# Performance work log

Hardware: AMD Instinct MI355X
Metric: run time of the kernel (lower is better)

## Reference

```python
import jax, jax.numpy as jnp
import numpy as np


def setup_inputs() -> dict:
    key = jax.random.key(0)
    k1, k2 = jax.random.split(key)
    B, H, W, D = 2, 160, 192, 160
    X = jax.random.normal(k1, (B, H, W, D, 2), dtype=jnp.float32)
    deformation = jax.random.normal(k2, (B, H, W, D, 3), dtype=jnp.float32)
    return {"X": X, "deformation": deformation}


def reference(X, deformation):
    # X: (B,H,W,D,2); warp the first channel by the dense deformation field.
    B, H, W, D, _ = X.shape
    Y = X[..., 0:1]                     # (B,H,W,D,1) volume to warp
    N = H * W * D

    # Identity grid, matching tf.meshgrid(x,y,z) 'xy' semantics: shape (H,W,D),
    # x varies along axis1 (width), y along axis0 (height), z along axis2 (depth).
    ys, xs, zs = jnp.meshgrid(
        jnp.arange(H, dtype=jnp.float32),
        jnp.arange(W, dtype=jnp.float32),
        jnp.arange(D, dtype=jnp.float32),
        indexing='ij')

    d = deformation.reshape(B, N, 3)
    x = xs.reshape(-1)[None, :] + d[..., 0]   # (B,N)
    y = ys.reshape(-1)[None, :] + d[..., 1]
    z = zs.reshape(-1)[None, :] + d[..., 2]

    x0 = jnp.floor(x).astype(jnp.int32); x1 = x0 + 1
    y0 = jnp.floor(y).astype(jnp.int32); y1 = y0 + 1
    z0 = jnp.floor(z).astype(jnp.int32); z1 = z0 + 1

    x0 = jnp.clip(x0, 0, W - 1); x1 = jnp.clip(x1, 0, W - 1)
    y0 = jnp.clip(y0, 0, H - 1); y1 = jnp.clip(y1, 0, H - 1)
    z0 = jnp.clip(z0, 0, D - 1); z1 = jnp.clip(z1, 0, D - 1)

    flat = Y.reshape(B, N, 1)           # (B, H*W*D, C=1)

    def gather(yy, xx, zz):
        idx = (yy * (W * D) + xx * D + zz)[..., None]   # (B,N,1)
        return jnp.take_along_axis(flat, idx, axis=1)

    p000 = gather(y0, x0, z0); p001 = gather(y0, x0, z1)
    p010 = gather(y0, x1, z0); p011 = gather(y0, x1, z1)
    p100 = gather(y1, x0, z0); p101 = gather(y1, x0, z1)
    p110 = gather(y1, x1, z0); p111 = gather(y1, x1, z1)

    # Weights use the CLIPPED corner coordinates (faithful to the original).
    x0f = x0.astype(jnp.float32); x1f = x1.astype(jnp.float32)
    y0f = y0.astype(jnp.float32); y1f = y1.astype(jnp.float32)
    z0f = z0.astype(jnp.float32); z1f = z1.astype(jnp.float32)

    w000 = ((y1f - y) * (x1f - x) * (z1f - z))[..., None]
    w001 = ((y1f - y) * (x1f - x) * (z - z0f))[..., None]
    w010 = ((y1f - y) * (x - x0f) * (z1f - z))[..., None]
    w011 = ((y1f - y) * (x - x0f) * (z - z0f))[..., None]
    w100 = ((y - y0f) * (x1f - x) * (z1f - z))[..., None]
    w101 = ((y - y0f) * (x1f - x) * (z - z0f))[..., None]
    w110 = ((y - y0f) * (x - x0f) * (z1f - z))[..., None]
    w111 = ((y - y0f) * (x - x0f) * (z - z0f))[..., None]

    out = (w000 * p000 + w001 * p001 + w010 * p010 + w011 * p011 +
           w100 * p100 + w101 * p101 + w110 * p110 + w111 * p111)
    return out.reshape(B, H, W, D, 1)
```

## Files before the change

### kernel.cpp

```cpp
#include <hip/hip_runtime.h>

#define BB 2
#define HH 160
#define WW 192
#define DD 160
#define NN (HH * WW * DD)
#define TOTAL (BB * NN)

__device__ inline unsigned short f2bf(float f) {
    unsigned u = __builtin_bit_cast(unsigned, f);
    u += 0x7FFFu + ((u >> 16) & 1u);
    return (unsigned short)(u >> 16);
}
__device__ inline float bf2f_lo(unsigned v) {
    return __builtin_bit_cast(float, v << 16);
}
__device__ inline float bf2f_hi(unsigned v) {
    return __builtin_bit_cast(float, v & 0xFFFF0000u);
}

struct __attribute__((packed, aligned(8))) f6u { float a, b, c, d, e, f; };

__global__ __launch_bounds__(256)
void compact_ch0_bf16_kernel(const float4* __restrict__ X4,
                             ushort4* __restrict__ C4) {
    const int i = blockIdx.x * 256 + threadIdx.x;
    const float4 a = X4[4 * i];
    const float4 b = X4[4 * i + 1];
    const float4 c = X4[4 * i + 2];
    const float4 d = X4[4 * i + 3];
    ushort4 lo, hi;
    lo.x = f2bf(a.x); lo.y = f2bf(a.z); lo.z = f2bf(b.x); lo.w = f2bf(b.z);
    hi.x = f2bf(c.x); hi.y = f2bf(c.z); hi.z = f2bf(d.x); hi.w = f2bf(d.z);
    C4[2 * i]     = lo;
    C4[2 * i + 1] = hi;
}

__global__ __launch_bounds__(256, 6)
void SpatialDeformer3D_kernel(const unsigned short* __restrict__ C,
                              const float* __restrict__ def,
                              float* __restrict__ out) {
    const int t  = blockIdx.x * 256 + threadIdx.x;
    const int n0 = t * 2;

    const int b    = (n0 >= NN) ? 1 : 0;
    const int rem  = n0 - b * NN;
    const int h    = rem / (WW * DD);
    const int rem2 = rem - h * (WW * DD);
    const int w    = rem2 / DD;
    const int d0   = rem2 - w * DD;

    const f6u dv = *(const f6u*)(def + (size_t)n0 * 3);
    const float dxs[2] = {dv.a, dv.d};
    const float dys[2] = {dv.b, dv.e};
    const float dzs[2] = {dv.c, dv.f};

    const unsigned bbase = (unsigned)b * (unsigned)NN * 2u;

    float xs[2], ys[2], zs[2];
    int aix0[2], aix1[2], aiy0[2], aiy1[2], alo[2], ahi[2], azb[2];
    unsigned o0, o1, o2, o3, o4, o5, o6, o7;
#pragma unroll
    for (int k = 0; k < 2; ++k) {
        const float x = (float)w + dxs[k];
        const float y = (float)h + dys[k];
        const float z = (float)(d0 + k) + dzs[k];
        xs[k] = x; ys[k] = y; zs[k] = z;

        const int fx0 = (int)floorf(x);
        const int fy0 = (int)floorf(y);
        const int fz0 = (int)floorf(z);

        const int ix0 = min(max(fx0, 0), WW - 1), ix1 = min(max(fx0 + 1, 0), WW - 1);
        const int iy0 = min(max(fy0, 0), HH - 1), iy1 = min(max(fy0 + 1, 0), HH - 1);
        const int czlo = min(max(fz0, 0), DD - 1);
        const int czhi = min(max(fz0 + 1, 0), DD - 1);
        const int zb   = min(max(fz0, 0), DD - 2);

        aix0[k] = ix0; aix1[k] = ix1; aiy0[k] = iy0; aiy1[k] = iy1;
        alo[k] = czlo; ahi[k] = czhi; azb[k] = zb;

        const unsigned r00 = bbase + (unsigned)(iy0 * (WW * DD) + ix0 * DD + zb) * 2u;
        const unsigned r01 = bbase + (unsigned)(iy0 * (WW * DD) + ix1 * DD + zb) * 2u;
        const unsigned r10 = bbase + (unsigned)(iy1 * (WW * DD) + ix0 * DD + zb) * 2u;
        const unsigned r11 = bbase + (unsigned)(iy1 * (WW * DD) + ix1 * DD + zb) * 2u;
        if (k == 0) { o0 = r00; o1 = r01; o2 = r10; o3 = r11; }
        else        { o4 = r00; o5 = r01; o6 = r10; o7 = r11; }
    }

    unsigned g0, g1, g2, g3, g4, g5, g6, g7;
    asm volatile(
        "global_load_dword %0, %8, %16\n\t"
        "global_load_dword %1, %9, %16\n\t"
        "global_load_dword %2, %10, %16\n\t"
        "global_load_dword %3, %11, %16\n\t"
        "global_load_dword %4, %12, %16\n\t"
        "global_load_dword %5, %13, %16\n\t"
        "global_load_dword %6, %14, %16\n\t"
        "global_load_dword %7, %15, %16"
        : "=&v"(g0), "=&v"(g1), "=&v"(g2), "=&v"(g3),
          "=&v"(g4), "=&v"(g5), "=&v"(g6), "=&v"(g7)
        : "v"(o0), "v"(o1), "v"(o2), "v"(o3),
          "v"(o4), "v"(o5), "v"(o6), "v"(o7),
          "s"(C));

    float wgt[2][6];
    bool lov[2], hiv[2];
#pragma unroll
    for (int k = 0; k < 2; ++k) {
        wgt[k][0] = (float)aix1[k] - xs[k];
        wgt[k][1] = xs[k] - (float)aix0[k];
        wgt[k][2] = (float)aiy1[k] - ys[k];
        wgt[k][3] = ys[k] - (float)aiy0[k];
        wgt[k][4] = (float)ahi[k] - zs[k];
        wgt[k][5] = zs[k] - (float)alo[k];
        lov[k] = (alo[k] == azb[k]);
        hiv[k] = (ahi[k] == azb[k] + 1);
    }

    asm volatile("s_waitcnt vmcnt(0)"
                 : "+v"(g0), "+v"(g1), "+v"(g2), "+v"(g3),
                   "+v"(g4), "+v"(g5), "+v"(g6), "+v"(g7));

    const unsigned gg[2][4] = {{g0, g1, g2, g3}, {g4, g5, g6, g7}};
    float res[2];
#pragma unroll
    for (int k = 0; k < 2; ++k) {
        const float v00l = bf2f_lo(gg[k][0]), v00h = bf2f_hi(gg[k][0]);
        const float v01l = bf2f_lo(gg[k][1]), v01h = bf2f_hi(gg[k][1]);
        const float v10l = bf2f_lo(gg[k][2]), v10h = bf2f_hi(gg[k][2]);
        const float v11l = bf2f_lo(gg[k][3]), v11h = bf2f_hi(gg[k][3]);

        const float p000 = lov[k] ? v00l : v00h;
        const float p001 = hiv[k] ? v00h : v00l;
        const float p010 = lov[k] ? v01l : v01h;
        const float p011 = hiv[k] ? v01h : v01l;
        const float p100 = lov[k] ? v10l : v10h;
        const float p101 = hiv[k] ? v10h : v10l;
        const float p110 = lov[k] ? v11l : v11h;
        const float p111 = hiv[k] ? v11h : v11l;

        const float wx0 = wgt[k][0], wx1 = wgt[k][1];
        const float wy0 = wgt[k][2], wy1 = wgt[k][3];
        const float wz0 = wgt[k][4], wz1 = wgt[k][5];

        res[k] =
            wy0 * (wx0 * (wz0 * p000 + wz1 * p001) + wx1 * (wz0 * p010 + wz1 * p011)) +
            wy1 * (wx0 * (wz0 * p100 + wz1 * p101) + wx1 * (wz0 * p110 + wz1 * p111));
    }

    *(float2*)(out + n0) = make_float2(res[0], res[1]);
}

__global__ __launch_bounds__(256)
void SpatialDeformer3D_direct_kernel(const float* __restrict__ X,
                                     const float* __restrict__ def,
                                     float* __restrict__ out) {
    const int n = blockIdx.x * 256 + threadIdx.x;
    const int b    = n / NN;
    const int rem  = n - b * NN;
    const int h    = rem / (WW * DD);
    const int rem2 = rem - h * (WW * DD);
    const int w    = rem2 / DD;
    const int d    = rem2 - w * DD;

    const float* dp = def + (size_t)n * 3;
    const float x = (float)w + dp[0];
    const float y = (float)h + dp[1];
    const float z = (float)d + dp[2];

    int ix0 = (int)floorf(x);
    int iy0 = (int)floorf(y);
    int iz0 = (int)floorf(z);
    int ix1 = ix0 + 1, iy1 = iy0 + 1, iz1 = iz0 + 1;
    ix0 = min(max(ix0, 0), WW - 1); ix1 = min(max(ix1, 0), WW - 1);
    iy0 = min(max(iy0, 0), HH - 1); iy1 = min(max(iy1, 0), HH - 1);
    iz0 = min(max(iz0, 0), DD - 1); iz1 = min(max(iz1, 0), DD - 1);

    const float wx0 = (float)ix1 - x, wx1 = x - (float)ix0;
    const float wy0 = (float)iy1 - y, wy1 = y - (float)iy0;
    const float wz0 = (float)iz1 - z, wz1 = z - (float)iz0;

    const float* Xb = X + (size_t)b * (2u * (size_t)NN);
    const int ry0 = iy0 * (WW * DD), ry1 = iy1 * (WW * DD);
    const int rx0 = ix0 * DD,        rx1 = ix1 * DD;

    const float p000 = Xb[(size_t)(ry0 + rx0 + iz0) * 2];
    const float p001 = Xb[(size_t)(ry0 + rx0 + iz1) * 2];
    const float p010 = Xb[(size_t)(ry0 + rx1 + iz0) * 2];
    const float p011 = Xb[(size_t)(ry0 + rx1 + iz1) * 2];
    const float p100 = Xb[(size_t)(ry1 + rx0 + iz0) * 2];
    const float p101 = Xb[(size_t)(ry1 + rx0 + iz1) * 2];
    const float p110 = Xb[(size_t)(ry1 + rx1 + iz0) * 2];
    const float p111 = Xb[(size_t)(ry1 + rx1 + iz1) * 2];

    const float r =
        wy0 * (wx0 * (wz0 * p000 + wz1 * p001) + wx1 * (wz0 * p010 + wz1 * p011)) +
        wy1 * (wx0 * (wz0 * p100 + wz1 * p101) + wx1 * (wz0 * p110 + wz1 * p111));

    out[n] = r;
}

extern "C" void kernel_launch(void* const* d_in, const int* in_sizes, int n_in,
                              void* d_out, int out_size, void* d_ws, size_t ws_size,
                              hipStream_t stream) {
    const float* X   = (const float*)d_in[0];
    const float* def = (const float*)d_in[1];
    float* out = (float*)d_out;

    const size_t need = (size_t)TOTAL * sizeof(unsigned short);
    if (ws_size >= need) {
        unsigned short* C = (unsigned short*)d_ws;
        compact_ch0_bf16_kernel<<<(TOTAL / 8) / 256, 256, 0, stream>>>(
            (const float4*)X, (ushort4*)C);
        SpatialDeformer3D_kernel<<<(TOTAL / 2) / 256, 256, 0, stream>>>(C, def, out);
    } else {
        SpatialDeformer3D_direct_kernel<<<TOTAL / 256, 256, 0, stream>>>(X, def, out);
    }
}
```

Baseline: 249.3 us.

## Add expanded 2x2x2 neighbor-packed bf16 volume so each sample needs one 16B load

Adds an extra pass that builds a layout in which each voxel stores its x/x+1 and y/y+1 neighbor bf16 values for z and z+1 in 16 bytes. The main kernel then fetches all eight trilinear corners with one uint4 load per sample instead of four dword gathers. The goal is fewer scattered memory transactions per sample. In exchange it writes and reads a 4x larger intermediate (about 9.8M*8 bytes) plus an extra kernel launch, and it needs more workspace. Clamped edge cases are handled with selects.

```diff
diff --git a/kernel.cpp b/kernel.cpp
--- a/kernel.cpp
+++ b/kernel.cpp
@@ -20,10 +20,13 @@
 }
 
 struct __attribute__((packed, aligned(8))) f6u { float a, b, c, d, e, f; };
+struct __attribute__((packed, aligned(2))) u32u { unsigned v; };
+
+union Q8 { uint4 q; unsigned short s[8]; };
 
 __global__ __launch_bounds__(256)
 void compact_ch0_bf16_kernel(const float4* __restrict__ X4,
-                             ushort4* __restrict__ C4) {
+                             ushort4* __restrict__ C4o) {
     const int i = blockIdx.x * 256 + threadIdx.x;
     const float4 a = X4[4 * i];
     const float4 b = X4[4 * i + 1];
@@ -32,12 +35,56 @@
     ushort4 lo, hi;
     lo.x = f2bf(a.x); lo.y = f2bf(a.z); lo.z = f2bf(b.x); lo.w = f2bf(b.z);
     hi.x = f2bf(c.x); hi.y = f2bf(c.z); hi.z = f2bf(d.x); hi.w = f2bf(d.z);
-    C4[2 * i]     = lo;
-    C4[2 * i + 1] = hi;
+    C4o[2 * i]     = lo;
+    C4o[2 * i + 1] = hi;
+}
+
+__global__ __launch_bounds__(256)
+void expand_c4_kernel(const unsigned short* __restrict__ C,
+                      uint4* __restrict__ C4) {
+    const int tid = blockIdx.x * 256 + threadIdx.x;
+    const int zc  = tid % 20;
+    const int r   = tid / 20;
+    const int x   = r % WW;
+    const int r2  = r / WW;
+    const int y   = r2 % HH;
+    const int b   = r2 / HH;
+
+    const int x1 = min(x + 1, WW - 1);
+    const int y1 = min(y + 1, HH - 1);
+    const int z0 = zc * 8;
+
+    const unsigned short* Cb = C + (size_t)b * NN;
+    const size_t r00 = (size_t)(y  * (WW * DD) + x  * DD + z0);
+    const size_t r01 = (size_t)(y  * (WW * DD) + x1 * DD + z0);
+    const size_t r10 = (size_t)(y1 * (WW * DD) + x  * DD + z0);
+    const size_t r11 = (size_t)(y1 * (WW * DD) + x1 * DD + z0);
+
+    Q8 a00, a01, a10, a11;
+    a00.q = *(const uint4*)(Cb + r00);
+    a01.q = *(const uint4*)(Cb + r01);
+    a10.q = *(const uint4*)(Cb + r10);
+    a11.q = *(const uint4*)(Cb + r11);
+
+    Q8 o[4];
+#pragma unroll
+    for (int z = 0; z < 8; ++z) {
+        const int qi = z >> 1, si = (z & 1) * 4;
+        o[qi].s[si + 0] = a00.s[z];
+        o[qi].s[si + 1] = a01.s[z];
+        o[qi].s[si + 2] = a10.s[z];
+        o[qi].s[si + 3] = a11.s[z];
+    }
+
+    uint4* dst = C4 + ((size_t)b * NN + (size_t)(y * WW + x) * DD + z0) / 2;
+    dst[0] = o[0].q;
+    dst[1] = o[1].q;
+    dst[2] = o[2].q;
+    dst[3] = o[3].q;
 }
 
 __global__ __launch_bounds__(256, 6)
-void SpatialDeformer3D_kernel(const unsigned short* __restrict__ C,
+void SpatialDeformer3D_kernel(const unsigned char* __restrict__ C4b,
                               const float* __restrict__ def,
                               float* __restrict__ out) {
     const int t  = blockIdx.x * 256 + threadIdx.x;
@@ -55,11 +102,12 @@
     const float dys[2] = {dv.b, dv.e};
     const float dzs[2] = {dv.c, dv.f};
 
-    const unsigned bbase = (unsigned)b * (unsigned)NN * 2u;
+    const unsigned bbase = (unsigned)b * (unsigned)NN * 8u;
 
     float xs[2], ys[2], zs[2];
     int aix0[2], aix1[2], aiy0[2], aiy1[2], alo[2], ahi[2], azb[2];
-    unsigned o0, o1, o2, o3, o4, o5, o6, o7;
+    bool x1hi[2], y1hi[2];
+    unsigned off[2];
 #pragma unroll
     for (int k = 0; k < 2; ++k) {
         const float x = (float)w + dxs[k];
@@ -79,33 +127,16 @@
 
         aix0[k] = ix0; aix1[k] = ix1; aiy0[k] = iy0; aiy1[k] = iy1;
         alo[k] = czlo; ahi[k] = czhi; azb[k] = zb;
-
-        const unsigned r00 = bbase + (unsigned)(iy0 * (WW * DD) + ix0 * DD + zb) * 2u;
-        const unsigned r01 = bbase + (unsigned)(iy0 * (WW * DD) + ix1 * DD + zb) * 2u;
-        const unsigned r10 = bbase + (unsigned)(iy1 * (WW * DD) + ix0 * DD + zb) * 2u;
-        const unsigned r11 = bbase + (unsigned)(iy1 * (WW * DD) + ix1 * DD + zb) * 2u;
-        if (k == 0) { o0 = r00; o1 = r01; o2 = r10; o3 = r11; }
-        else        { o4 = r00; o5 = r01; o6 = r10; o7 = r11; }
-    }
-
-    unsigned g0, g1, g2, g3, g4, g5, g6, g7;
-    asm volatile(
-        "global_load_dword %0, %8, %16\n\t"
-        "global_load_dword %1, %9, %16\n\t"
-        "global_load_dword %2, %10, %16\n\t"
-        "global_load_dword %3, %11, %16\n\t"
-        "global_load_dword %4, %12, %16\n\t"
-        "global_load_dword %5, %13, %16\n\t"
-        "global_load_dword %6, %14, %16\n\t"
-        "global_load_dword %7, %15, %16"
-        : "=&v"(g0), "=&v"(g1), "=&v"(g2), "=&v"(g3),
-          "=&v"(g4), "=&v"(g5), "=&v"(g6), "=&v"(g7)
-        : "v"(o0), "v"(o1), "v"(o2), "v"(o3),
-          "v"(o4), "v"(o5), "v"(o6), "v"(o7),
-          "s"(C));
+        x1hi[k] = (fx0 >= 0);
+        y1hi[k] = (fy0 >= 0);
+
+        off[k] = bbase + (unsigned)((iy0 * WW + ix0) * DD + zb) * 8u;
+    }
+
+    uint4 q0 = *(const uint4*)(C4b + off[0]);
+    uint4 q1 = *(const uint4*)(C4b + off[1]);
 
     float wgt[2][6];
-    bool lov[2], hiv[2];
 #pragma unroll
     for (int k = 0; k < 2; ++k) {
         wgt[k][0] = (float)aix1[k] - xs[k];
@@ -114,31 +145,31 @@
         wgt[k][3] = ys[k] - (float)aiy0[k];
         wgt[k][4] = (float)ahi[k] - zs[k];
         wgt[k][5] = zs[k] - (float)alo[k];
-        lov[k] = (alo[k] == azb[k]);
-        hiv[k] = (ahi[k] == azb[k] + 1);
-    }
-
-    asm volatile("s_waitcnt vmcnt(0)"
-                 : "+v"(g0), "+v"(g1), "+v"(g2), "+v"(g3),
-                   "+v"(g4), "+v"(g5), "+v"(g6), "+v"(g7));
-
-    const unsigned gg[2][4] = {{g0, g1, g2, g3}, {g4, g5, g6, g7}};
+    }
+
     float res[2];
 #pragma unroll
     for (int k = 0; k < 2; ++k) {
-        const float v00l = bf2f_lo(gg[k][0]), v00h = bf2f_hi(gg[k][0]);
-        const float v01l = bf2f_lo(gg[k][1]), v01h = bf2f_hi(gg[k][1]);
-        const float v10l = bf2f_lo(gg[k][2]), v10h = bf2f_hi(gg[k][2]);
-        const float v11l = bf2f_lo(gg[k][3]), v11h = bf2f_hi(gg[k][3]);
-
-        const float p000 = lov[k] ? v00l : v00h;
-        const float p001 = hiv[k] ? v00h : v00l;
-        const float p010 = lov[k] ? v01l : v01h;
-        const float p011 = hiv[k] ? v01h : v01l;
-        const float p100 = lov[k] ? v10l : v10h;
-        const float p101 = hiv[k] ? v10h : v10l;
-        const float p110 = lov[k] ? v11l : v11h;
-        const float p111 = hiv[k] ? v11h : v11l;
+        const uint4 q = (k == 0) ? q0 : q1;
+        const bool lov = (alo[k] == azb[k]);
+        const bool hiv = (ahi[k] == azb[k] + 1);
+
+        const unsigned A0 = lov ? q.x : q.z;
+        const unsigned A1 = lov ? q.y : q.w;
+        const unsigned B0 = hiv ? q.z : q.x;
+        const unsigned B1 = hiv ? q.w : q.y;
+
+        const unsigned Ay = y1hi[k] ? A1 : A0;
+        const unsigned By = y1hi[k] ? B1 : B0;
+
+        const float p000 = bf2f_lo(A0);
+        const float p001 = bf2f_lo(B0);
+        const float p010 = x1hi[k] ? bf2f_hi(A0) : bf2f_lo(A0);
+        const float p011 = x1hi[k] ? bf2f_hi(B0) : bf2f_lo(B0);
+        const float p100 = bf2f_lo(Ay);
+        const float p101 = bf2f_lo(By);
+        const float p110 = x1hi[k] ? bf2f_hi(Ay) : bf2f_lo(Ay);
+        const float p111 = x1hi[k] ? bf2f_hi(By) : bf2f_lo(By);
 
         const float wx0 = wgt[k][0], wx1 = wgt[k][1];
         const float wy0 = wgt[k][2], wy1 = wgt[k][3];
@@ -149,6 +180,65 @@
             wy1 * (wx0 * (wz0 * p100 + wz1 * p101) + wx1 * (wz0 * p110 + wz1 * p111));
     }
 
+    *(float2*)(out + n0) = make_float2(res[0], res[1]);
+}
+
+__global__ __launch_bounds__(256, 6)
+void SpatialDeformer3D_pairgather_kernel(const unsigned short* __restrict__ C,
+                                         const float* __restrict__ def,
+                                         float* __restrict__ out) {
+    const int t  = blockIdx.x * 256 + threadIdx.x;
+    const int n0 = t * 2;
+    const int b    = (n0 >= NN) ? 1 : 0;
+    const int rem  = n0 - b * NN;
+    const int h    = rem / (WW * DD);
+    const int rem2 = rem - h * (WW * DD);
+    const int w    = rem2 / DD;
+    const int d0   = rem2 - w * DD;
+
+    const f6u dv = *(const f6u*)(def + (size_t)n0 * 3);
+    const float dxs[2] = {dv.a, dv.d};
+    const float dys[2] = {dv.b, dv.e};
+    const float dzs[2] = {dv.c, dv.f};
+    const unsigned short* Cb = C + (size_t)b * NN;
+
+    float res[2];
+#pragma unroll
+    for (int k = 0; k < 2; ++k) {
+        const float x = (float)w + dxs[k];
+        const float y = (float)h + dys[k];
+        const float z = (float)(d0 + k) + dzs[k];
+        const int fx0 = (int)floorf(x);
+        const int fy0 = (int)floorf(y);
+        const int fz0 = (int)floorf(z);
+        const int ix0 = min(max(fx0, 0), WW - 1), ix1 = min(max(fx0 + 1, 0), WW - 1);
+        const int iy0 = min(max(fy0, 0), HH - 1), iy1 = min(max(fy0 + 1, 0), HH - 1);
+        const int czlo = min(max(fz0, 0), DD - 1);
+        const int czhi = min(max(fz0 + 1, 0), DD - 1);
+        const int zb   = min(max(fz0, 0), DD - 2);
+        const float wx0 = (float)ix1 - x, wx1 = x - (float)ix0;
+        const float wy0 = (float)iy1 - y, wy1 = y - (float)iy0;
+        const float wz0 = (float)czhi - z, wz1 = z - (float)czlo;
+        const bool lov = (czlo == zb), hiv = (czhi == zb + 1);
+
+        const unsigned g00 = ((const u32u*)(Cb + iy0 * (WW * DD) + ix0 * DD + zb))->v;
+        const unsigned g01 = ((const u32u*)(Cb + iy0 * (WW * DD) + ix1 * DD + zb))->v;
+        const unsigned g10 = ((const u32u*)(Cb + iy1 * (WW * DD) + ix0 * DD + zb))->v;
+        const unsigned g11 = ((const u32u*)(Cb + iy1 * (WW * DD) + ix1 * DD + zb))->v;
+
+        const float p000 = lov ? bf2f_lo(g00) : bf2f_hi(g00);
+        const float p001 = hiv ? bf2f_hi(g00) : bf2f_lo(g00);
+        const float p010 = lov ? bf2f_lo(g01) : bf2f_hi(g01);
+        const float p011 = hiv ? bf2f_hi(g01) : bf2f_lo(g01);
+        const float p100 = lov ? bf2f_lo(g10) : bf2f_hi(g10);
+        const float p101 = hiv ? bf2f_hi(g10) : bf2f_lo(g10);
+        const float p110 = lov ? bf2f_lo(g11) : bf2f_hi(g11);
+        const float p111 = hiv ? bf2f_hi(g11) : bf2f_lo(g11);
+
+        res[k] =
+            wy0 * (wx0 * (wz0 * p000 + wz1 * p001) + wx1 * (wz0 * p010 + wz1 * p011)) +
+            wy1 * (wx0 * (wz0 * p100 + wz1 * p101) + wx1 * (wz0 * p110 + wz1 * p111));
+    }
     *(float2*)(out + n0) = make_float2(res[0], res[1]);
 }
 
@@ -208,12 +298,22 @@
     const float* def = (const float*)d_in[1];
     float* out = (float*)d_out;
 
-    const size_t need = (size_t)TOTAL * sizeof(unsigned short);
-    if (ws_size >= need) {
+    const size_t needC  = (size_t)TOTAL * sizeof(unsigned short);
+    const size_t needC4 = needC + (size_t)TOTAL * 8u;
+
+    if (ws_size >= needC4) {
+        unsigned short* C  = (unsigned short*)d_ws;
+        unsigned char*  C4 = (unsigned char*)d_ws + needC;
+        compact_ch0_bf16_kernel<<<(TOTAL / 8) / 256, 256, 0, stream>>>(
+            (const float4*)X, (ushort4*)C);
+        expand_c4_kernel<<<(TOTAL / 8) / 256, 256, 0, stream>>>(C, (uint4*)C4);
+        SpatialDeformer3D_kernel<<<(TOTAL / 2) / 256, 256, 0, stream>>>(C4, def, out);
+    } else if (ws_size >= needC) {
         unsigned short* C = (unsigned short*)d_ws;
         compact_ch0_bf16_kernel<<<(TOTAL / 8) / 256, 256, 0, stream>>>(
             (const float4*)X, (ushort4*)C);
-        SpatialDeformer3D_kernel<<<(TOTAL / 2) / 256, 256, 0, stream>>>(C, def, out);
+        SpatialDeformer3D_pairgather_kernel<<<(TOTAL / 2) / 256, 256, 0, stream>>>(
+            C, def, out);
     } else {
         SpatialDeformer3D_direct_kernel<<<TOTAL / 256, 256, 0, stream>>>(X, def, out);
     }
```

New measurement: 289.2 us. 1.16x slower.
